# Kernel tuning notes

Measured on AMD Instinct MI355X. Metric: run time of the kernel, lower is better.

## Reference

```python
import jax, jax.numpy as jnp
import numpy as np

B, Z, H, T = 256, 512, 1024, 512   # batch, z_size, hidden (conductor==decoder), num_tokens
L, N = 16, 16                      # num_levels, notes_per_bar


def setup_inputs() -> dict:
    key = jax.random.key(0)
    ks = jax.random.split(key, 16)
    s = 0.05  # weight init scale
    rn = lambda k, shp, sc=1.0: sc * jax.random.normal(k, shp, dtype=jnp.float32)
    return {
        "z": rn(ks[0], (B, L * N, 1, Z)),
        "dec_h0": rn(ks[1], (L, B, H)),
        "dec_c0": rn(ks[2], (L, B, H)),
        # linear_in (computed but unused by the original forward)
        "lin_in_W": rn(ks[3], (Z, Z), s), "lin_in_b": rn(ks[4], (Z,), s),
        # conductor LSTM (input Z -> hidden H), PyTorch gate order i,f,g,o
        "cond_Wih": rn(ks[5], (4 * H, Z), s), "cond_Whh": rn(ks[6], (4 * H, H), s),
        "cond_bih": rn(ks[7], (4 * H,), s), "cond_bhh": rn(ks[8], (4 * H,), s),
        # decoder LSTM (input T+H -> hidden H)
        "dec_Wih": rn(ks[9], (4 * H, T + H), s), "dec_Whh": rn(ks[10], (4 * H, H), s),
        "dec_bih": rn(ks[11], (4 * H,), s), "dec_bhh": rn(ks[12], (4 * H,), s),
        # output projection
        "out_W": rn(ks[13], (T, H), s), "out_b": rn(ks[14], (T,), s),
    }


def _lstm_cell(x, h, c, Wih, Whh, b):
    gates = x @ Wih.T + h @ Whh.T + b            # [B, 4H]
    i, f, g, o = jnp.split(gates, 4, axis=-1)
    c = jax.nn.sigmoid(f) * c + jax.nn.sigmoid(i) * jnp.tanh(g)
    h = jax.nn.sigmoid(o) * jnp.tanh(c)
    return h, c


def reference(z, dec_h0, dec_c0, lin_in_W, lin_in_b,
              cond_Wih, cond_Whh, cond_bih, cond_bhh,
              dec_Wih, dec_Whh, dec_bih, dec_bhh, out_W, out_b):
    Bsz = z.shape[0]
    Tt = out_b.shape[0]
    Hh = cond_Whh.shape[1]

    _unused = z @ lin_in_W.T + lin_in_b  # linear_in output is discarded in the source

    cond_b = cond_bih + cond_bhh
    dec_b = dec_bih + dec_bhh

    # conductor consumes z[:, L*level, 0, :] for each level
    z_lv = jnp.transpose(z[:, jnp.arange(L) * L, 0, :], (1, 0, 2))  # [L, B, Z]

    def level_step(carry, xs):
        ch, cc = carry
        zl, dh, dc = xs
        ch, cc = _lstm_cell(zl, ch, cc, cond_Wih, cond_Whh, cond_b)
        emb = ch  # [B, H], fixed conductor embedding for this bar

        def note_step(c2, _):
            note, dh2, dc2 = c2
            inp = jnp.concatenate([emb, note], axis=-1)  # [B, H+T]
            dh2, dc2 = _lstm_cell(inp, dh2, dc2, dec_Wih, dec_Whh, dec_b)
            out = jax.nn.sigmoid(dh2 @ out_W.T + out_b)  # [B, T]
            return (out, dh2, dc2), out

        note0 = jnp.zeros((Bsz, Tt), dtype=z.dtype)
        _, outs = jax.lax.scan(note_step, (note0, dh, dc), None, length=N)  # [N, B, T]
        return (ch, cc), outs

    h0 = jnp.zeros((Bsz, Hh), dtype=z.dtype)
    _, all_outs = jax.lax.scan(level_step, (h0, h0), (z_lv, dec_h0, dec_c0))  # [L, N, B, T]
    notes = jnp.transpose(all_outs, (2, 0, 1, 3)).reshape(Bsz, L * N, Tt)
    return notes
```

## Files before the change

### kernel.cpp

```cpp
#include <hip/hip_runtime.h>

typedef __bf16 bf16;
typedef __attribute__((ext_vector_type(8))) __bf16 bf16x8;
typedef __attribute__((ext_vector_type(4))) float f32x4;
typedef __attribute__((ext_vector_type(4))) unsigned short u16x4;

__device__ __forceinline__ void gload_lds16(const void* g, void* l) {
  __builtin_amdgcn_global_load_lds(
      (const __attribute__((address_space(1))) void*)g,
      (__attribute__((address_space(3))) void*)l, 16, 0, 0);
}

__device__ __forceinline__ float sigmoidf_(float x) { return 1.0f / (1.0f + expf(-x)); }

__device__ __forceinline__ float bf2f(unsigned short u) {
  union { unsigned int i; float f; } v;
  v.i = ((unsigned int)u) << 16;
  return v.f;
}
__device__ __forceinline__ unsigned short f2bfbits(float x) {
  union { bf16 b; unsigned short u; } v;
  v.b = (bf16)x;
  return v.u;
}

#define SB() __builtin_amdgcn_sched_barrier(0)
#define BAR()                          \
  do {                                 \
    SB();                              \
    __builtin_amdgcn_s_barrier();      \
    SB();                              \
  } while (0)

#define MFMA16(a, b, c) __builtin_amdgcn_mfma_f32_16x16x32_bf16(a, b, c, 0, 0, 0)

template<int MODE>
__global__ __launch_bounds__(512, 2)
void gemm8(const bf16* __restrict__ A, int lda,
           const bf16* __restrict__ Bw, int K,
           bf16* __restrict__ Cb,
           const bf16* __restrict__ X, const float* __restrict__ bias,
           float* __restrict__ cst, bf16* __restrict__ hout, int ldh) {
  extern __shared__ __align__(16) char smem_raw[];
  bf16* lsA = (bf16*)smem_raw;
  bf16* lsB = lsA + 2 * 16384;

  const int tid = threadIdx.x;
  const int lane = tid & 63;
  const int wave = tid >> 6;
  const int wm = wave >> 2, wn = wave & 3;

  const int bid = blockIdx.x;
  const int wgid = (bid & 7) * 32 + (bid >> 3);
  const int m0 = (wgid >> 4) * 256, n0 = (wgid & 15) * 256;

  const int nkt = K >> 6;

  const int srow = tid >> 3;
  const int csw = ((tid & 7) * 8) ^ ((srow & 7) << 3);
  const bf16* gA = A + (size_t)m0 * lda + csw;
  const bf16* gB = Bw + (size_t)n0 * K + csw;

  auto stageA = [&](int kt, int h) {
    bf16* d = lsA + (kt & 1) * 16384 + h * 8192 + tid * 8;
    const bf16* s = gA + (size_t)(h * 128 + srow) * lda + (size_t)kt * 64;
    gload_lds16(s, d);
    gload_lds16(s + (size_t)64 * lda, d + 4096);
  };
  auto stageB = [&](int kt, int h) {
    bf16* d = lsB + (kt & 1) * 16384 + h * 8192 + tid * 8;
    const bf16* s = gB + (size_t)(h * 128 + srow) * K + (size_t)kt * 64;
    gload_lds16(s, d);
    gload_lds16(s + (size_t)64 * K, d + 4096);
  };

  const int c0 = ((lane >> 4) * 8) ^ ((lane & 7) << 3);
  const int c1 = c0 ^ 32;
  const int abase = (wm * 128 + (lane & 15)) * 64;
  const int bbase = (wn * 64 + (lane & 15)) * 64;

  f32x4 acc[8][4] = {};

  stageA(0, 0); stageA(0, 1); stageB(0, 0); stageB(0, 1);
  if (nkt > 1) {
    stageB(1, 0);
    asm volatile("s_waitcnt vmcnt(2)" ::: "memory");
  } else {
    asm volatile("s_waitcnt vmcnt(0)" ::: "memory");
  }
  BAR();

  for (int u = 0; u < nkt; ++u) {
    const int cb = u & 1;
    const bf16* pA = lsA + cb * 16384;
    const bf16* pB = lsB + cb * 16384;
    bf16x8 av[4], bv[4];

#pragma unroll
    for (int f = 0; f < 4; ++f) av[f] = *(const bf16x8*)&pA[abase + f * 1024 + c0];
#pragma unroll
    for (int g = 0; g < 4; ++g) bv[g] = *(const bf16x8*)&pB[bbase + g * 1024 + c0];
    if (u + 1 < nkt) { stageA(u + 1, 0); stageB(u + 1, 1); }
    BAR();
    __builtin_amdgcn_s_setprio(1);
#pragma unroll
    for (int f = 0; f < 4; ++f)
#pragma unroll
      for (int g = 0; g < 4; ++g)
        acc[f][g] = MFMA16(av[f], bv[g], acc[f][g]);
    __builtin_amdgcn_s_setprio(0);
    BAR();

    {
      bf16x8 a1[4];
#pragma unroll
      for (int f = 0; f < 4; ++f) a1[f] = *(const bf16x8*)&pA[abase + (f + 4) * 1024 + c0];
      if (u + 1 < nkt) stageA(u + 1, 1);
      BAR();
      __builtin_amdgcn_s_setprio(1);
#pragma unroll
      for (int f = 0; f < 4; ++f)
#pragma unroll
        for (int g = 0; g < 4; ++g)
          acc[f + 4][g] = MFMA16(a1[f], bv[g], acc[f + 4][g]);
      __builtin_amdgcn_s_setprio(0);
      BAR();
    }

#pragma unroll
    for (int f = 0; f < 4; ++f) av[f] = *(const bf16x8*)&pA[abase + f * 1024 + c1];
#pragma unroll
    for (int g = 0; g < 4; ++g) bv[g] = *(const bf16x8*)&pB[bbase + g * 1024 + c1];
    BAR();
    __builtin_amdgcn_s_setprio(1);
#pragma unroll
    for (int f = 0; f < 4; ++f)
#pragma unroll
      for (int g = 0; g < 4; ++g)
        acc[f][g] = MFMA16(av[f], bv[g], acc[f][g]);
    __builtin_amdgcn_s_setprio(0);
    BAR();

    {
      bf16x8 a1[4];
#pragma unroll
      for (int f = 0; f < 4; ++f) a1[f] = *(const bf16x8*)&pA[abase + (f + 4) * 1024 + c1];
      if (u + 2 < nkt) {
        stageB(u + 2, 0);
        SB();
        asm volatile("s_waitcnt vmcnt(2)" ::: "memory");
      } else {
        SB();
        asm volatile("s_waitcnt vmcnt(0)" ::: "memory");
      }
      BAR();
      __builtin_amdgcn_s_setprio(1);
#pragma unroll
      for (int f = 0; f < 4; ++f)
#pragma unroll
        for (int g = 0; g < 4; ++g)
          acc[f + 4][g] = MFMA16(a1[f], bv[g], acc[f + 4][g]);
      __builtin_amdgcn_s_setprio(0);
      BAR();
    }
  }

  const int jj = lane & 15;
  const int rb = m0 + wm * 128 + ((lane >> 4) << 2);
  const int q = (n0 >> 6) + wn;
  if constexpr (MODE == 0) {
#pragma unroll
    for (int f = 0; f < 8; ++f)
#pragma unroll
      for (int r = 0; r < 4; ++r) {
        u16x4 pk;
        pk[0] = f2bfbits(acc[f][0][r]);
        pk[1] = f2bfbits(acc[f][1][r]);
        pk[2] = f2bfbits(acc[f][2][r]);
        pk[3] = f2bfbits(acc[f][3][r]);
        *(u16x4*)&Cb[(size_t)(rb + f * 16 + r) * 4096 + q * 64 + jj * 4] = pk;
      }
  } else {
    const int j = q * 16 + jj;
    const f32x4 bq = *(const f32x4*)&bias[q * 64 + jj * 4];
#pragma unroll
    for (int f = 0; f < 8; ++f) {
#pragma unroll
      for (int r = 0; r < 4; ++r) {
        const int row = rb + f * 16 + r;
        const u16x4 xv = *(const u16x4*)&X[(size_t)row * 4096 + q * 64 + jj * 4];
        const float gi = acc[f][0][r] + bf2f(xv[0]) + bq[0];
        const float gf = acc[f][1][r] + bf2f(xv[1]) + bq[1];
        const float gg = acc[f][2][r] + bf2f(xv[2]) + bq[2];
        const float go = acc[f][3][r] + bf2f(xv[3]) + bq[3];
        const size_t ci = (size_t)row * 1024 + j;
        const float cn = sigmoidf_(gf) * cst[ci] + sigmoidf_(gi) * tanhf(gg);
        cst[ci] = cn;
        hout[(size_t)row * ldh + j] = (bf16)(sigmoidf_(go) * tanhf(cn));
      }
    }
  }
}

template<int BM, int BN, int WM, int WN, int MODE>
__global__ __launch_bounds__(WM * WN * 64)
void gemm_bt(const bf16* __restrict__ A, int lda,
             const bf16* __restrict__ Bw, int ldb,
             float* __restrict__ C, int ldc, int K,
             const float* __restrict__ outb, float* __restrict__ dout,
             bf16* __restrict__ anote, int nstep) {
  constexpr int BK = 64;
  constexpr int THREADS = WM * WN * 64;
  constexpr int SM = BM / WM, SN = BN / WN;
  constexpr int FM = SM / 16, FN = SN / 16;

  __shared__ __align__(16) bf16 lsA[BM * BK];
  __shared__ __align__(16) bf16 lsB[BN * BK];

  const int tid = threadIdx.x;
  const int lane = tid & 63;
  const int wave = tid >> 6;
  const int wm = wave / WN, wn = wave % WN;
  const int m0 = blockIdx.y * BM;
  const int n0 = blockIdx.x * BN;

  f32x4 acc[FM][FN] = {};

  const bf16* gA = A + (size_t)m0 * lda;
  const bf16* gB = Bw + (size_t)n0 * ldb;

  for (int k0 = 0; k0 < K; k0 += BK) {
#pragma unroll
    for (int i = 0; i < (BM * 8) / THREADS; ++i) {
      int idx = i * THREADS + tid;
      gload_lds16(gA + (size_t)(idx >> 3) * lda + k0 + (idx & 7) * 8, &lsA[idx * 8]);
    }
#pragma unroll
    for (int i = 0; i < (BN * 8) / THREADS; ++i) {
      int idx = i * THREADS + tid;
      gload_lds16(gB + (size_t)(idx >> 3) * ldb + k0 + (idx & 7) * 8, &lsB[idx * 8]);
    }
    __syncthreads();

#pragma unroll
    for (int kk = 0; kk < BK; kk += 32) {
      bf16x8 av[FM], bv[FN];
#pragma unroll
      for (int i = 0; i < FM; ++i)
        av[i] = *(const bf16x8*)&lsA[(wm * SM + i * 16 + (lane & 15)) * BK + kk + (lane >> 4) * 8];
#pragma unroll
      for (int j = 0; j < FN; ++j)
        bv[j] = *(const bf16x8*)&lsB[(wn * SN + j * 16 + (lane & 15)) * BK + kk + (lane >> 4) * 8];
#pragma unroll
      for (int i = 0; i < FM; ++i)
#pragma unroll
        for (int j = 0; j < FN; ++j)
          acc[i][j] = MFMA16(av[i], bv[j], acc[i][j]);
    }
    __syncthreads();
  }

#pragma unroll
  for (int i = 0; i < FM; ++i) {
#pragma unroll
    for (int j = 0; j < FN; ++j) {
      const int col = n0 + wn * SN + j * 16 + (lane & 15);
      const int rbase = m0 + wm * SM + i * 16 + ((lane >> 4) << 2);
#pragma unroll
      for (int r = 0; r < 4; ++r) {
        const int row = rbase + r;
        float v = acc[i][j][r];
        if constexpr (MODE == 0) {
          C[(size_t)row * ldc + col] = v;
        } else {
          v = sigmoidf_(v + outb[col]);
          const int l = row >> 8, b = row & 255;
          dout[((size_t)(b * 256 + l * 16 + nstep)) * 512 + col] = v;
          anote[(size_t)row * 1536 + col] = (bf16)v;
        }
      }
    }
  }
}

template<int BM, int BJ, int WM, int WJ>
__global__ __launch_bounds__(WM * WJ * 64, 2)
void gemm_cell(const bf16* __restrict__ A, int lda,
               const bf16* __restrict__ Bw,
               const bf16* __restrict__ X,
               const float* __restrict__ bias,
               float* __restrict__ cst,
               bf16* __restrict__ hout, int ldh, int K) {
  constexpr int BK = 64;
  constexpr int THREADS = WM * WJ * 64;
  constexpr int BN = BJ * 64;
  constexpr int SM = BM / WM;
  constexpr int TJ = BJ / WJ;
  constexpr int FM = SM / 16;

  __shared__ __align__(16) bf16 lsA[BM * BK];
  __shared__ __align__(16) bf16 lsB[BN * BK];

  const int tid = threadIdx.x;
  const int lane = tid & 63;
  const int wave = tid >> 6;
  const int wm = wave / WJ, wj = wave % WJ;
  const int m0 = blockIdx.y * BM;
  const int qb = blockIdx.x * BJ;

  f32x4 acc[FM][TJ][4] = {};

  const bf16* gA = A + (size_t)m0 * lda;
  const bf16* gB = Bw + (size_t)(qb * 64) * K;

  for (int k0 = 0; k0 < K; k0 += BK) {
#pragma unroll
    for (int i = 0; i < (BM * 8) / THREADS; ++i) {
      int idx = i * THREADS + tid;
      gload_lds16(gA + (size_t)(idx >> 3) * lda + k0 + (idx & 7) * 8, &lsA[idx * 8]);
    }
#pragma unroll
    for (int i = 0; i < (BN * 8) / THREADS; ++i) {
      int idx = i * THREADS + tid;
      gload_lds16(gB + (size_t)(idx >> 3) * K + k0 + (idx & 7) * 8, &lsB[idx * 8]);
    }
    __syncthreads();

#pragma unroll
    for (int kk = 0; kk < BK; kk += 32) {
      bf16x8 av[FM], bv[TJ][4];
#pragma unroll
      for (int i = 0; i < FM; ++i)
        av[i] = *(const bf16x8*)&lsA[(wm * SM + i * 16 + (lane & 15)) * BK + kk + (lane >> 4) * 8];
#pragma unroll
      for (int t = 0; t < TJ; ++t)
#pragma unroll
        for (int g = 0; g < 4; ++g)
          bv[t][g] = *(const bf16x8*)
              &lsB[((wj * TJ + t) * 64 + g * 16 + (lane & 15)) * BK + kk + (lane >> 4) * 8];
#pragma unroll
      for (int i = 0; i < FM; ++i)
#pragma unroll
        for (int t = 0; t < TJ; ++t)
#pragma unroll
          for (int g = 0; g < 4; ++g)
            acc[i][t][g] = MFMA16(av[i], bv[t][g], acc[i][t][g]);
    }
    __syncthreads();
  }

#pragma unroll
  for (int i = 0; i < FM; ++i) {
#pragma unroll
    for (int t = 0; t < TJ; ++t) {
      const int q = qb + wj * TJ + t;
      const int jj = lane & 15;
      const int j = q * 16 + jj;
      const int rbase = m0 + wm * SM + i * 16 + ((lane >> 4) << 2);
      const f32x4 bq = *(const f32x4*)&bias[q * 64 + jj * 4];
#pragma unroll
      for (int r = 0; r < 4; ++r) {
        const int row = rbase + r;
        const u16x4 xv = *(const u16x4*)&X[(size_t)row * 4096 + q * 64 + jj * 4];
        const float gi = acc[i][t][0][r] + bf2f(xv[0]) + bq[0];
        const float gf = acc[i][t][1][r] + bf2f(xv[1]) + bq[1];
        const float gg = acc[i][t][2][r] + bf2f(xv[2]) + bq[2];
        const float go = acc[i][t][3][r] + bf2f(xv[3]) + bq[3];
        const size_t ci = (size_t)row * 1024 + j;
        const float c = sigmoidf_(gf) * cst[ci] + sigmoidf_(gi) * tanhf(gg);
        cst[ci] = c;
        hout[(size_t)row * ldh + j] = (bf16)(sigmoidf_(go) * tanhf(c));
      }
    }
  }
}


__global__ void conv_f32_bf16(const float* __restrict__ src, bf16* __restrict__ dst, int n) {
  int idx = blockIdx.x * 256 + threadIdx.x;
  if (idx < n) dst[idx] = (bf16)src[idx];
}

__device__ __forceinline__ int p_src_row(int n) {
  int q = n >> 6, gate = (n >> 4) & 3, jj = n & 15;
  return gate * 1024 + q * 16 + jj;
}

__global__ void pack_w_dec(const float* __restrict__ wih, const float* __restrict__ whh,
                           bf16* __restrict__ dst) {
  int idx = blockIdx.x * 256 + threadIdx.x;
  int n = idx / 1536, c = idx - n * 1536;
  int r = p_src_row(n);
  float v = (c < 512) ? wih[(size_t)r * 1536 + 1024 + c] : whh[(size_t)r * 1024 + (c - 512)];
  dst[idx] = (bf16)v;
}

__global__ void pack_w_emb(const float* __restrict__ wih, bf16* __restrict__ dst) {
  int idx = blockIdx.x * 256 + threadIdx.x;
  int n = idx >> 10, c = idx & 1023;
  dst[idx] = (bf16)wih[(size_t)p_src_row(n) * 1536 + c];
}

__global__ void pack_w_perm(const float* __restrict__ src, bf16* __restrict__ dst, int Kw) {
  int idx = blockIdx.x * 256 + threadIdx.x;
  int n = idx / Kw, c = idx - n * Kw;
  dst[idx] = (bf16)src[(size_t)p_src_row(n) * Kw + c];
}

__global__ void pack_bias(const float* __restrict__ bih, const float* __restrict__ bhh,
                          float* __restrict__ dst) {
  int n = blockIdx.x * 256 + threadIdx.x;
  int q = n >> 6, jj = (n >> 2) & 15, g = n & 3;
  int r = g * 1024 + q * 16 + jj;
  dst[n] = bih[r] + bhh[r];
}

__global__ void pack_zb(const float* __restrict__ z, bf16* __restrict__ dst) {
  int idx = blockIdx.x * 256 + threadIdx.x;
  int m = idx >> 9, k = idx & 511;
  int l = m >> 8, b = m & 255;
  dst[idx] = (bf16)z[((size_t)b * 256 + 16 * l) * 512 + k];
}

__global__ void init_cond(float* __restrict__ cc, bf16* __restrict__ hz0) {
  int idx = blockIdx.x * 256 + threadIdx.x;
  cc[idx] = 0.f;
  hz0[idx] = (bf16)0.f;
}

__global__ void init_state(const float* __restrict__ h0, const float* __restrict__ c0,
                           bf16* __restrict__ Abuf, float* __restrict__ cdec) {
  int idx = blockIdx.x * 256 + threadIdx.x;
  int m = idx / 1536, c = idx - m * 1536;
  if (c < 512) {
    Abuf[idx] = (bf16)0.f;
  } else {
    int j = c - 512;
    size_t s = (size_t)m * 1024 + j;
    Abuf[idx] = (bf16)h0[s];
    cdec[s] = c0[s];
  }
}

extern "C" void kernel_launch(void* const* d_in, const int* in_sizes, int n_in,
                              void* d_out, int out_size, void* d_ws, size_t ws_size,
                              hipStream_t stream) {
  const float* z        = (const float*)d_in[0];
  const float* dec_h0   = (const float*)d_in[1];
  const float* dec_c0   = (const float*)d_in[2];
  const float* cond_Wih = (const float*)d_in[5];
  const float* cond_Whh = (const float*)d_in[6];
  const float* cond_bih = (const float*)d_in[7];
  const float* cond_bhh = (const float*)d_in[8];
  const float* dec_Wih  = (const float*)d_in[9];
  const float* dec_Whh  = (const float*)d_in[10];
  const float* dec_bih  = (const float*)d_in[11];
  const float* dec_bhh  = (const float*)d_in[12];
  const float* out_W    = (const float*)d_in[13];
  const float* out_b    = (const float*)d_in[14];
  float* out = (float*)d_out;

  char* ws = (char*)d_ws;
  size_t off = 0;
  auto alloc = [&](size_t bytes) {
    void* p = ws + off;
    off += (bytes + 255) & ~(size_t)255;
    return p;
  };
  bf16* E     = (bf16*)alloc(4096ull * 4096 * 2);
  bf16* Xz    = (bf16*)alloc(4096ull * 4096 * 2);
  float* cdec = (float*)alloc(4096ull * 1024 * 4);
  bf16* Abuf  = (bf16*)alloc(4096ull * 1536 * 2);
  bf16* Wd    = (bf16*)alloc(4096ull * 1536 * 2);
  bf16* We    = (bf16*)alloc(4096ull * 1024 * 2);
  bf16* Wcih  = (bf16*)alloc(4096ull * 512 * 2);
  bf16* Wchh  = (bf16*)alloc(4096ull * 1024 * 2);
  bf16* Wo    = (bf16*)alloc(512ull * 1024 * 2);
  float* cc   = (float*)alloc(256ull * 1024 * 4);
  bf16* emb   = (bf16*)alloc(4096ull * 1024 * 2);
  bf16* Zb    = (bf16*)alloc(4096ull * 512 * 2);
  bf16* hz0   = (bf16*)alloc(256ull * 1024 * 2);
  float* bdP  = (float*)alloc(4096ull * 4);
  float* bcP  = (float*)alloc(4096ull * 4);

  dim3 b256(256);

  hipFuncSetAttribute(reinterpret_cast<const void*>(&gemm8<0>),
                      hipFuncAttributeMaxDynamicSharedMemorySize, 131072);
  hipFuncSetAttribute(reinterpret_cast<const void*>(&gemm8<1>),
                      hipFuncAttributeMaxDynamicSharedMemorySize, 131072);

  pack_w_perm<<<4096 * 512 / 256, b256, 0, stream>>>(cond_Wih, Wcih, 512);
  pack_w_perm<<<4096 * 1024 / 256, b256, 0, stream>>>(cond_Whh, Wchh, 1024);
  conv_f32_bf16<<<(512 * 1024 + 255) / 256, b256, 0, stream>>>(out_W, Wo, 512 * 1024);
  pack_w_dec<<<4096 * 1536 / 256, b256, 0, stream>>>(dec_Wih, dec_Whh, Wd);
  pack_w_emb<<<4096 * 1024 / 256, b256, 0, stream>>>(dec_Wih, We);
  pack_bias<<<16, b256, 0, stream>>>(dec_bih, dec_bhh, bdP);
  pack_bias<<<16, b256, 0, stream>>>(cond_bih, cond_bhh, bcP);
  pack_zb<<<4096 * 512 / 256, b256, 0, stream>>>(z, Zb);
  init_cond<<<256 * 1024 / 256, b256, 0, stream>>>(cc, hz0);
  init_state<<<4096 * 1536 / 256, b256, 0, stream>>>(dec_h0, dec_c0, Abuf, cdec);

  gemm8<0><<<256, 512, 131072, stream>>>(Zb, 512, Wcih, 512, Xz,
                                         nullptr, nullptr, nullptr, nullptr, 0);

  for (int l = 0; l < 16; ++l) {
    const bf16* hprev = (l == 0) ? hz0 : (emb + (size_t)(l - 1) * 256 * 1024);
    gemm_cell<32, 2, 2, 2><<<dim3(32, 8), dim3(256), 0, stream>>>(
        hprev, 1024, Wchh, Xz + (size_t)l * 256 * 4096, bcP,
        cc, emb + (size_t)l * 256 * 1024, 1024, 1024);
  }

  gemm8<0><<<256, 512, 131072, stream>>>(emb, 1024, We, 1024, E,
                                         nullptr, nullptr, nullptr, nullptr, 0);

  for (int n = 0; n < 16; ++n) {
    gemm8<1><<<256, 512, 131072, stream>>>(Abuf, 1536, Wd, 1536, nullptr,
                                           E, bdP, cdec, Abuf + 512, 1536);
    gemm_bt<128, 64, 2, 2, 1><<<dim3(512 / 64, 4096 / 128), dim3(256), 0, stream>>>(
        Abuf + 512, 1536, Wo, 1024, nullptr, 0, 1024, out_b, out, Abuf, n);
  }
}
```

Measured before the change: 1.758 ms.

## Restructure gemm8 k-loop to prefetch two k-tiles and ping-pong decoder state buffers

The gemm8 main loop now works on pairs of k-tiles. Both LDS buffers are filled in the prologue, and A/B fragments for both k-halves are loaded at once, with the B tile split into two column halves. Next-tile global→LDS staging is spread across four MFMA phases, using explicit lgkmcnt/vmcnt waits. The aim is more overlap between loads and MFMA and fewer stalls between barriers, at the cost of higher register pressure and the assumption that nkt is even. Separately, the decoder state buffer is double-buffered so each step reads one copy and writes the next, which removes a read/write overlap on the hidden-state columns.

```diff
diff --git a/kernel.cpp b/kernel.cpp
--- a/kernel.cpp
+++ b/kernel.cpp
@@ -30,6 +30,11 @@
     SB();                              \
     __builtin_amdgcn_s_barrier();      \
     SB();                              \
+  } while (0)
+#define LGKM0()                                          \
+  do {                                                   \
+    asm volatile("s_waitcnt lgkmcnt(0)" ::: "memory");   \
+    SB();                                                \
   } while (0)
 
 #define MFMA16(a, b, c) __builtin_amdgcn_mfma_f32_16x16x32_bf16(a, b, c, 0, 0, 0)
@@ -82,87 +87,167 @@
   f32x4 acc[8][4] = {};
 
   stageA(0, 0); stageA(0, 1); stageB(0, 0); stageB(0, 1);
-  if (nkt > 1) {
-    stageB(1, 0);
-    asm volatile("s_waitcnt vmcnt(2)" ::: "memory");
-  } else {
-    asm volatile("s_waitcnt vmcnt(0)" ::: "memory");
-  }
+  stageA(1, 0); stageA(1, 1); stageB(1, 0); stageB(1, 1);
+  asm volatile("s_waitcnt vmcnt(8)" ::: "memory");
   BAR();
 
-  for (int u = 0; u < nkt; ++u) {
-    const int cb = u & 1;
-    const bf16* pA = lsA + cb * 16384;
-    const bf16* pB = lsB + cb * 16384;
-    bf16x8 av[4], bv[4];
-
-#pragma unroll
-    for (int f = 0; f < 4; ++f) av[f] = *(const bf16x8*)&pA[abase + f * 1024 + c0];
-#pragma unroll
-    for (int g = 0; g < 4; ++g) bv[g] = *(const bf16x8*)&pB[bbase + g * 1024 + c0];
-    if (u + 1 < nkt) { stageA(u + 1, 0); stageB(u + 1, 1); }
-    BAR();
-    __builtin_amdgcn_s_setprio(1);
-#pragma unroll
-    for (int f = 0; f < 4; ++f)
-#pragma unroll
-      for (int g = 0; g < 4; ++g)
-        acc[f][g] = MFMA16(av[f], bv[g], acc[f][g]);
-    __builtin_amdgcn_s_setprio(0);
-    BAR();
-
-    {
-      bf16x8 a1[4];
-#pragma unroll
-      for (int f = 0; f < 4; ++f) a1[f] = *(const bf16x8*)&pA[abase + (f + 4) * 1024 + c0];
-      if (u + 1 < nkt) stageA(u + 1, 1);
-      BAR();
-      __builtin_amdgcn_s_setprio(1);
-#pragma unroll
-      for (int f = 0; f < 4; ++f)
-#pragma unroll
-        for (int g = 0; g < 4; ++g)
-          acc[f + 4][g] = MFMA16(a1[f], bv[g], acc[f + 4][g]);
-      __builtin_amdgcn_s_setprio(0);
-      BAR();
-    }
-
-#pragma unroll
-    for (int f = 0; f < 4; ++f) av[f] = *(const bf16x8*)&pA[abase + f * 1024 + c1];
-#pragma unroll
-    for (int g = 0; g < 4; ++g) bv[g] = *(const bf16x8*)&pB[bbase + g * 1024 + c1];
-    BAR();
-    __builtin_amdgcn_s_setprio(1);
-#pragma unroll
-    for (int f = 0; f < 4; ++f)
-#pragma unroll
-      for (int g = 0; g < 4; ++g)
-        acc[f][g] = MFMA16(av[f], bv[g], acc[f][g]);
-    __builtin_amdgcn_s_setprio(0);
-    BAR();
-
-    {
-      bf16x8 a1[4];
-#pragma unroll
-      for (int f = 0; f < 4; ++f) a1[f] = *(const bf16x8*)&pA[abase + (f + 4) * 1024 + c1];
-      if (u + 2 < nkt) {
-        stageB(u + 2, 0);
-        SB();
-        asm volatile("s_waitcnt vmcnt(2)" ::: "memory");
-      } else {
-        SB();
-        asm volatile("s_waitcnt vmcnt(0)" ::: "memory");
-      }
-      BAR();
-      __builtin_amdgcn_s_setprio(1);
-#pragma unroll
-      for (int f = 0; f < 4; ++f)
-#pragma unroll
-        for (int g = 0; g < 4; ++g)
-          acc[f + 4][g] = MFMA16(a1[f], bv[g], acc[f + 4][g]);
-      __builtin_amdgcn_s_setprio(0);
-      BAR();
-    }
+  for (int t = 0; t < nkt; t += 2) {
+    const bool pre = (t + 2 < nkt);
+    const bf16* pA0 = lsA;
+    const bf16* pB0 = lsB;
+    const bf16* pA1 = lsA + 16384;
+    const bf16* pB1 = lsB + 16384;
+
+    bf16x8 aA[4][2], aB[4][2], bA[2][2], bB[2][2];
+
+#pragma unroll
+    for (int f = 0; f < 4; ++f) {
+      aA[f][0] = *(const bf16x8*)&pA0[abase + f * 1024 + c0];
+      aA[f][1] = *(const bf16x8*)&pA0[abase + f * 1024 + c1];
+    }
+#pragma unroll
+    for (int g = 0; g < 2; ++g) {
+      bA[g][0] = *(const bf16x8*)&pB0[bbase + g * 1024 + c0];
+      bA[g][1] = *(const bf16x8*)&pB0[bbase + g * 1024 + c1];
+    }
+    BAR();
+    LGKM0();
+    __builtin_amdgcn_s_setprio(1);
+#pragma unroll
+    for (int s = 0; s < 2; ++s)
+#pragma unroll
+      for (int f = 0; f < 4; ++f)
+#pragma unroll
+        for (int g = 0; g < 2; ++g)
+          acc[f][g] = MFMA16(aA[f][s], bA[g][s], acc[f][g]);
+    __builtin_amdgcn_s_setprio(0);
+    BAR();
+
+#pragma unroll
+    for (int f = 0; f < 4; ++f) {
+      aB[f][0] = *(const bf16x8*)&pA0[abase + (f + 4) * 1024 + c0];
+      aB[f][1] = *(const bf16x8*)&pA0[abase + (f + 4) * 1024 + c1];
+    }
+#pragma unroll
+    for (int g = 0; g < 2; ++g) {
+      bB[g][0] = *(const bf16x8*)&pB0[bbase + (g + 2) * 1024 + c0];
+      bB[g][1] = *(const bf16x8*)&pB0[bbase + (g + 2) * 1024 + c1];
+    }
+    BAR();
+    LGKM0();
+    __builtin_amdgcn_s_setprio(1);
+#pragma unroll
+    for (int s = 0; s < 2; ++s)
+#pragma unroll
+      for (int f = 0; f < 4; ++f)
+#pragma unroll
+        for (int g = 0; g < 2; ++g)
+          acc[f + 4][g] = MFMA16(aB[f][s], bA[g][s], acc[f + 4][g]);
+    __builtin_amdgcn_s_setprio(0);
+    BAR();
+
+    if (pre) stageA(t + 2, 0);
+    BAR();
+    __builtin_amdgcn_s_setprio(1);
+#pragma unroll
+    for (int s = 0; s < 2; ++s)
+#pragma unroll
+      for (int f = 0; f < 4; ++f)
+#pragma unroll
+        for (int g = 0; g < 2; ++g)
+          acc[f][g + 2] = MFMA16(aA[f][s], bB[g][s], acc[f][g + 2]);
+    __builtin_amdgcn_s_setprio(0);
+    BAR();
+
+    if (pre) stageA(t + 2, 1);
+    SB();
+    __builtin_amdgcn_s_setprio(1);
+#pragma unroll
+    for (int s = 0; s < 2; ++s)
+#pragma unroll
+      for (int f = 0; f < 4; ++f)
+#pragma unroll
+        for (int g = 0; g < 2; ++g)
+          acc[f + 4][g + 2] = MFMA16(aB[f][s], bB[g][s], acc[f + 4][g + 2]);
+    __builtin_amdgcn_s_setprio(0);
+    if (pre) asm volatile("s_waitcnt vmcnt(4)" ::: "memory");
+    else     asm volatile("s_waitcnt vmcnt(0)" ::: "memory");
+    BAR();
+
+#pragma unroll
+    for (int f = 0; f < 4; ++f) {
+      aA[f][0] = *(const bf16x8*)&pA1[abase + f * 1024 + c0];
+      aA[f][1] = *(const bf16x8*)&pA1[abase + f * 1024 + c1];
+    }
+#pragma unroll
+    for (int g = 0; g < 2; ++g) {
+      bA[g][0] = *(const bf16x8*)&pB1[bbase + g * 1024 + c0];
+      bA[g][1] = *(const bf16x8*)&pB1[bbase + g * 1024 + c1];
+    }
+    if (pre) stageB(t + 2, 0);
+    BAR();
+    LGKM0();
+    __builtin_amdgcn_s_setprio(1);
+#pragma unroll
+    for (int s = 0; s < 2; ++s)
+#pragma unroll
+      for (int f = 0; f < 4; ++f)
+#pragma unroll
+        for (int g = 0; g < 2; ++g)
+          acc[f][g] = MFMA16(aA[f][s], bA[g][s], acc[f][g]);
+    __builtin_amdgcn_s_setprio(0);
+    BAR();
+
+#pragma unroll
+    for (int f = 0; f < 4; ++f) {
+      aB[f][0] = *(const bf16x8*)&pA1[abase + (f + 4) * 1024 + c0];
+      aB[f][1] = *(const bf16x8*)&pA1[abase + (f + 4) * 1024 + c1];
+    }
+#pragma unroll
+    for (int g = 0; g < 2; ++g) {
+      bB[g][0] = *(const bf16x8*)&pB1[bbase + (g + 2) * 1024 + c0];
+      bB[g][1] = *(const bf16x8*)&pB1[bbase + (g + 2) * 1024 + c1];
+    }
+    if (pre) stageB(t + 2, 1);
+    BAR();
+    LGKM0();
+    __builtin_amdgcn_s_setprio(1);
+#pragma unroll
+    for (int s = 0; s < 2; ++s)
+#pragma unroll
+      for (int f = 0; f < 4; ++f)
+#pragma unroll
+        for (int g = 0; g < 2; ++g)
+          acc[f + 4][g] = MFMA16(aB[f][s], bA[g][s], acc[f + 4][g]);
+    __builtin_amdgcn_s_setprio(0);
+    BAR();
+
+    if (pre) { stageA(t + 3, 0); stageA(t + 3, 1); }
+    BAR();
+    __builtin_amdgcn_s_setprio(1);
+#pragma unroll
+    for (int s = 0; s < 2; ++s)
+#pragma unroll
+      for (int f = 0; f < 4; ++f)
+#pragma unroll
+        for (int g = 0; g < 2; ++g)
+          acc[f][g + 2] = MFMA16(aA[f][s], bB[g][s], acc[f][g + 2]);
+    __builtin_amdgcn_s_setprio(0);
+    BAR();
+
+    if (pre) { stageB(t + 3, 0); stageB(t + 3, 1); }
+    SB();
+    __builtin_amdgcn_s_setprio(1);
+#pragma unroll
+    for (int s = 0; s < 2; ++s)
+#pragma unroll
+      for (int f = 0; f < 4; ++f)
+#pragma unroll
+        for (int g = 0; g < 2; ++g)
+          acc[f + 4][g + 2] = MFMA16(aB[f][s], bB[g][s], acc[f + 4][g + 2]);
+    __builtin_amdgcn_s_setprio(0);
+    if (pre) asm volatile("s_waitcnt vmcnt(8)" ::: "memory");
+    BAR();
   }
 
   const int jj = lane & 15;
@@ -470,7 +555,8 @@
   bf16* E     = (bf16*)alloc(4096ull * 4096 * 2);
   bf16* Xz    = (bf16*)alloc(4096ull * 4096 * 2);
   float* cdec = (float*)alloc(4096ull * 1024 * 4);
-  bf16* Abuf  = (bf16*)alloc(4096ull * 1536 * 2);
+  bf16* Ab0   = (bf16*)alloc(4096ull * 1536 * 2);
+  bf16* Ab1   = (bf16*)alloc(4096ull * 1536 * 2);
   bf16* Wd    = (bf16*)alloc(4096ull * 1536 * 2);
   bf16* We    = (bf16*)alloc(4096ull * 1024 * 2);
   bf16* Wcih  = (bf16*)alloc(4096ull * 512 * 2);
@@ -499,7 +585,7 @@
   pack_bias<<<16, b256, 0, stream>>>(cond_bih, cond_bhh, bcP);
   pack_zb<<<4096 * 512 / 256, b256, 0, stream>>>(z, Zb);
   init_cond<<<256 * 1024 / 256, b256, 0, stream>>>(cc, hz0);
-  init_state<<<4096 * 1536 / 256, b256, 0, stream>>>(dec_h0, dec_c0, Abuf, cdec);
+  init_state<<<4096 * 1536 / 256, b256, 0, stream>>>(dec_h0, dec_c0, Ab0, cdec);
 
   gemm8<0><<<256, 512, 131072, stream>>>(Zb, 512, Wcih, 512, Xz,
                                          nullptr, nullptr, nullptr, nullptr, 0);
@@ -515,9 +601,11 @@
                                          nullptr, nullptr, nullptr, nullptr, 0);
 
   for (int n = 0; n < 16; ++n) {
-    gemm8<1><<<256, 512, 131072, stream>>>(Abuf, 1536, Wd, 1536, nullptr,
-                                           E, bdP, cdec, Abuf + 512, 1536);
+    bf16* Sc = (n & 1) ? Ab1 : Ab0;
+    bf16* Sn = (n & 1) ? Ab0 : Ab1;
+    gemm8<1><<<256, 512, 131072, stream>>>(Sc, 1536, Wd, 1536, nullptr,
+                                           E, bdP, cdec, Sn + 512, 1536);
     gemm_bt<128, 64, 2, 2, 1><<<dim3(512 / 64, 4096 / 128), dim3(256), 0, stream>>>(
-        Abuf + 512, 1536, Wo, 1024, nullptr, 0, 1024, out_b, out, Abuf, n);
-  }
-}
+        Sn + 512, 1536, Wo, 1024, nullptr, 0, 1024, out_b, out, Sn, n);
+  }
+}
```

After: 3.176 ms. +80.7%, slower.
